# Performance work log

Measured on AMD Instinct MI355X. Metric: run time of the kernel, lower is better.

Reference implementation:

```python
import jax, jax.numpy as jnp
import numpy as np

EPS = 1e-6

def _quant_per_token(x):
    # dynamic per-token symmetric int8 quantization (simulated in float)
    s = jnp.max(jnp.abs(x), axis=-1, keepdims=True) / 127.0  # [T,1]
    q = jnp.clip(jnp.round(x / s), -127.0, 127.0)
    return q, s

def _quant_weight(W):
    # per-output-channel symmetric int8 weight quantization (W: [out,in])
    s = jnp.max(jnp.abs(W), axis=1, keepdims=True) / 127.0  # [out,1]
    q = jnp.round(W / s)
    return q, s

def _w8a8(qx, sx, W, b):
    # int8xint8 GEMM with per-token act scale and per-channel weight scale, fp out
    qw, sw = _quant_weight(W)
    return (qx @ qw.T) * (sx * sw.T) + b

def _rmsnorm_bias(x, w, b, eps=EPS):
    # RMSNormGeneral: x * rsqrt(mean(x^2)+eps) * w + b (no mean subtraction)
    var = jnp.mean(x * x, axis=-1, keepdims=True)
    return x * jax.lax.rsqrt(var + eps) * w + b

def setup_inputs() -> dict:
    key = jax.random.key(0)
    ks = jax.random.split(key, 16)
    E, H, F = 1280, 20, 5120
    B, S = 16, 1024
    T = B * S
    d = {
        'hidden': jax.random.normal(ks[0], (T, E), jnp.float32),
        'ln1_w': jax.random.uniform(ks[1], (E,), jnp.float32, 0.5, 1.5),
        'ln1_b': jax.random.normal(ks[2], (E,), jnp.float32) * 0.02,
        'ln2_w': jax.random.uniform(ks[3], (E,), jnp.float32, 0.5, 1.5),
        'ln2_b': jax.random.normal(ks[4], (E,), jnp.float32) * 0.02,
        'W_qkv': jax.random.normal(ks[5], (3 * E, E), jnp.float32) * 0.02,
        'b_qkv': jax.random.normal(ks[6], (3 * E,), jnp.float32) * 0.02,
        'W_out': jax.random.normal(ks[7], (E, E), jnp.float32) * 0.02,
        'b_out': jax.random.normal(ks[8], (E,), jnp.float32) * 0.02,
        'W_fc1': jax.random.normal(ks[9], (F, E), jnp.float32) * 0.02,
        'b_fc1': jax.random.normal(ks[10], (F,), jnp.float32) * 0.02,
        'W_fc2': jax.random.normal(ks[11], (E, F), jnp.float32) * 0.02,
        'b_fc2': jax.random.normal(ks[12], (E,), jnp.float32) * 0.02,
        'bsz': B,
        'seqlen': S,
    }
    return d

def reference(hidden, ln1_w, ln1_b, ln2_w, ln2_b, W_qkv, b_qkv, W_out, b_out,
              W_fc1, b_fc1, W_fc2, b_fc2, bsz, seqlen):
    E = hidden.shape[-1]
    H = 20
    hd = E // H

    # --- self-attention block ---
    residual = hidden
    y = _rmsnorm_bias(hidden, ln1_w, ln1_b)
    qx, sx = _quant_per_token(y)
    qkv = _w8a8(qx, sx, W_qkv, b_qkv)                      # [T, 3E]
    q, k, v = jnp.split(qkv, 3, axis=-1)
    q = q.reshape(bsz, seqlen, H, hd)
    k = k.reshape(bsz, seqlen, H, hd)
    v = v.reshape(bsz, seqlen, H, hd)
    scale = 1.0 / np.sqrt(hd)
    scores = jnp.einsum('bqhd,bkhd->bhqk', q, k) * scale   # non-causal
    probs = jax.nn.softmax(scores, axis=-1)
    attn = jnp.einsum('bhqk,bkhd->bqhd', probs, v).reshape(bsz * seqlen, E)
    qa, sa = _quant_per_token(attn)
    o = _w8a8(qa, sa, W_out, b_out)
    hidden = residual + o

    # --- MLP block ---
    residual = hidden
    y = _rmsnorm_bias(hidden, ln2_w, ln2_b)
    qx, sx = _quant_per_token(y)
    f1 = _w8a8(qx, sx, W_fc1, b_fc1)                       # [T, F]
    g = jax.nn.gelu(f1, approximate=False)                 # fused gelu_and_quant
    qg, sg = _quant_per_token(g)
    f2 = _w8a8(qg, sg, W_fc2, b_fc2)
    return residual + f2
```

## Files before the change

### kernel.cpp

```cpp
#include <hip/hip_runtime.h>
#include <hip/hip_bf16.h>
#include <stdint.h>

#define E_DIM 1280
#define F_DIM 5120
#define T_DIM 16384
#define B_SZ  16
#define S_LEN 1024
#define NH    20

typedef int v4i __attribute__((ext_vector_type(4)));
typedef __attribute__((ext_vector_type(8))) short v8s;
typedef __attribute__((ext_vector_type(4))) float v4f;

__device__ __forceinline__ float wred_sum(float v) {
#pragma unroll
  for (int m = 32; m > 0; m >>= 1) v += __shfl_xor(v, m, 64);
  return v;
}
__device__ __forceinline__ float wred_max(float v) {
#pragma unroll
  for (int m = 32; m > 0; m >>= 1) v = fmaxf(v, __shfl_xor(v, m, 64));
  return v;
}
__device__ __forceinline__ void gload_lds16(const void* g, void* l) {
  __builtin_amdgcn_global_load_lds((const __attribute__((address_space(1))) void*)g,
                                   (__attribute__((address_space(3))) void*)l, 16, 0, 0);
}

__global__ __launch_bounds__(256) void wquant_kernel(
    const float* __restrict__ W, int8_t* __restrict__ qw, float* __restrict__ sw, int K) {
  __shared__ float red[4];
  const int row = blockIdx.x;
  const int tid = threadIdx.x;
  const float* wr = W + (size_t)row * K;
  float amax = 0.f;
  for (int c = tid; c < K; c += 256) amax = fmaxf(amax, fabsf(wr[c]));
  amax = wred_max(amax);
  if ((tid & 63) == 0) red[tid >> 6] = amax;
  __syncthreads();
  amax = fmaxf(fmaxf(red[0], red[1]), fmaxf(red[2], red[3]));
  float sc = amax * (1.0f / 127.0f);
  if (tid == 0) sw[row] = sc;
  for (int c = tid; c < K; c += 256) {
    float qv = rintf(wr[c] / sc);
    qw[(size_t)row * K + c] = (int8_t)qv;
  }
}

__global__ __launch_bounds__(256) void rms_quant_kernel(
    const float* __restrict__ x, const float* __restrict__ w, const float* __restrict__ b,
    int8_t* __restrict__ q, float* __restrict__ s) {
  __shared__ float red[4];
  const int row = blockIdx.x;
  const int tid = threadIdx.x;
  const float* xr = x + (size_t)row * E_DIM;
  float vals[5];
  float ss = 0.f;
#pragma unroll
  for (int i = 0; i < 5; ++i) {
    float v = xr[tid + i * 256];
    vals[i] = v; ss += v * v;
  }
  ss = wred_sum(ss);
  if ((tid & 63) == 0) red[tid >> 6] = ss;
  __syncthreads();
  ss = red[0] + red[1] + red[2] + red[3];
  float rstd = rsqrtf(ss * (1.0f / E_DIM) + 1e-6f);
  float y[5]; float amax = 0.f;
#pragma unroll
  for (int i = 0; i < 5; ++i) {
    int c = tid + i * 256;
    float v = vals[i] * rstd * w[c] + b[c];
    y[i] = v;
    amax = fmaxf(amax, fabsf(v));
  }
  amax = wred_max(amax);
  __syncthreads();
  if ((tid & 63) == 0) red[tid >> 6] = amax;
  __syncthreads();
  amax = fmaxf(fmaxf(red[0], red[1]), fmaxf(red[2], red[3]));
  float sc = amax * (1.0f / 127.0f);
  if (tid == 0) s[row] = sc;
#pragma unroll
  for (int i = 0; i < 5; ++i) {
    int c = tid + i * 256;
    float qv = rintf(y[i] / sc);
    qv = fminf(fmaxf(qv, -127.f), 127.f);
    q[(size_t)row * E_DIM + c] = (int8_t)qv;
  }
}

__global__ __launch_bounds__(256) void row_quant_bf_kernel(
    const __hip_bfloat16* __restrict__ x, int8_t* __restrict__ q, float* __restrict__ s) {
  __shared__ float red[4];
  const int row = blockIdx.x;
  const int tid = threadIdx.x;
  const __hip_bfloat16* xr = x + (size_t)row * E_DIM;
  float vals[5]; float amax = 0.f;
#pragma unroll
  for (int i = 0; i < 5; ++i) {
    float v = __bfloat162float(xr[tid + i * 256]);
    vals[i] = v;
    amax = fmaxf(amax, fabsf(v));
  }
  amax = wred_max(amax);
  if ((tid & 63) == 0) red[tid >> 6] = amax;
  __syncthreads();
  amax = fmaxf(fmaxf(red[0], red[1]), fmaxf(red[2], red[3]));
  float sc = amax * (1.0f / 127.0f);
  if (tid == 0) s[row] = sc;
#pragma unroll
  for (int i = 0; i < 5; ++i) {
    int c = tid + i * 256;
    float qv = rintf(vals[i] / sc);
    qv = fminf(fmaxf(qv, -127.f), 127.f);
    q[(size_t)row * E_DIM + c] = (int8_t)qv;
  }
}

__global__ __launch_bounds__(256) void gelu_quant_kernel(
    const __hip_bfloat16* __restrict__ f1, int8_t* __restrict__ q, float* __restrict__ s) {
  __shared__ float red[4];
  const int row = blockIdx.x;
  const int tid = threadIdx.x;
  const __hip_bfloat16* xr = f1 + (size_t)row * F_DIM;
  float g[20]; float amax = 0.f;
#pragma unroll
  for (int i = 0; i < 20; ++i) {
    float v = __bfloat162float(xr[tid + i * 256]);
    float gv = 0.5f * v * (1.0f + erff(v * 0.70710678118654752440f));
    g[i] = gv;
    amax = fmaxf(amax, fabsf(gv));
  }
  amax = wred_max(amax);
  if ((tid & 63) == 0) red[tid >> 6] = amax;
  __syncthreads();
  amax = fmaxf(fmaxf(red[0], red[1]), fmaxf(red[2], red[3]));
  float sc = amax * (1.0f / 127.0f);
  if (tid == 0) s[row] = sc;
  int8_t* qr = q + (size_t)row * (2 * F_DIM);
#pragma unroll
  for (int i = 0; i < 20; ++i) {
    int c = tid + i * 256;
    float qv = rintf(g[i] / sc);
    qv = fminf(fmaxf(qv, -127.f), 127.f);
    qr[c] = (int8_t)qv;
  }
}

template <int MODE>
__global__ __launch_bounds__(256) void gemm_i8(
    const int8_t* __restrict__ A, const int8_t* __restrict__ B,
    const float* __restrict__ sx, const float* __restrict__ sw,
    const float* __restrict__ bias, const float* __restrict__ resid,
    void* __restrict__ outp, int M, int N, int K, int lda) {
  __shared__ __align__(16) int8_t Asl[128 * 64];
  __shared__ __align__(16) int8_t Bsl[128 * 64];
  const int tid = threadIdx.x;
  const int lane = tid & 63;
  const int wave = tid >> 6;
  const int wm = wave >> 1, wn = wave & 1;
  const int quad = lane >> 4;
  const int l16 = lane & 15;
  const int m0 = blockIdx.y * 128;
  const int n0 = blockIdx.x * 128;

  v4i acc[4][4];
#pragma unroll
  for (int i = 0; i < 4; ++i)
#pragma unroll
    for (int j = 0; j < 4; ++j) acc[i][j] = (v4i){0, 0, 0, 0};

  const int nk = K >> 6;
#pragma unroll 1
  for (int ks = 0; ks < nk; ++ks) {
    __syncthreads();
    const long k0 = (long)ks * 64;
#pragma unroll
    for (int issue = 0; issue < 2; ++issue) {
      int c = (issue * 4 + wave) * 64 + lane;
      int row = c >> 2;
      int scol = (c & 3) << 4;
      int gcol = scol ^ ((row & 3) << 4);
      gload_lds16(A + (long)(m0 + row) * lda + k0 + gcol, &Asl[c * 16]);
      gload_lds16(B + (long)(n0 + row) * K + k0 + gcol, &Bsl[c * 16]);
    }
    __syncthreads();
    v4i af[4], bf[4];
#pragma unroll
    for (int i = 0; i < 4; ++i) {
      int row = wm * 64 + i * 16 + l16;
      af[i] = *(const v4i*)&Asl[row * 64 + ((quad * 16) ^ ((row & 3) << 4))];
    }
#pragma unroll
    for (int j = 0; j < 4; ++j) {
      int row = wn * 64 + j * 16 + l16;
      bf[j] = *(const v4i*)&Bsl[row * 64 + ((quad * 16) ^ ((row & 3) << 4))];
    }
#pragma unroll
    for (int i = 0; i < 4; ++i)
#pragma unroll
      for (int j = 0; j < 4; ++j)
        acc[i][j] = __builtin_amdgcn_mfma_i32_16x16x64_i8(af[i], bf[j], acc[i][j], 0, 0, 0);
  }

  float swv[4], bv[4];
#pragma unroll
  for (int j = 0; j < 4; ++j) {
    int n = n0 + wn * 64 + j * 16 + l16;
    swv[j] = sw[n];
    bv[j] = bias[n];
  }
#pragma unroll
  for (int i = 0; i < 4; ++i) {
#pragma unroll
    for (int r = 0; r < 4; ++r) {
      int m = m0 + wm * 64 + i * 16 + quad * 4 + r;
      float sxm = sx[m];
#pragma unroll
      for (int j = 0; j < 4; ++j) {
        int n = n0 + wn * 64 + j * 16 + l16;
        float v = (float)acc[i][j][r] * (sxm * swv[j]) + bv[j];
        if constexpr (MODE == 0) {
          ((__hip_bfloat16*)outp)[(size_t)m * N + n] = __float2bfloat16(v);
        } else {
          ((float*)outp)[(size_t)m * N + n] = v + resid[(size_t)m * N + n];
        }
      }
    }
  }
}

__global__ __launch_bounds__(256) void vt_kernel(
    const __hip_bfloat16* __restrict__ qkv, __hip_bfloat16* __restrict__ Vt) {
  __shared__ __hip_bfloat16 tile[64][72];
  const int bh = blockIdx.y, kc = blockIdx.x;
  const int b = bh / NH, h = bh % NH;
  const int tid = threadIdx.x;
  const size_t base = ((size_t)b * S_LEN + (size_t)kc * 64) * (3 * E_DIM) + 2 * E_DIM + h * 64;
#pragma unroll
  for (int i = 0; i < 2; ++i) {
    int idx = tid + i * 256;
    int row = idx >> 3, c8 = (idx & 7) * 8;
    *(uint4*)&tile[row][c8] = *(const uint4*)(qkv + base + (size_t)row * (3 * E_DIM) + c8);
  }
  __syncthreads();
#pragma unroll
  for (int i = 0; i < 2; ++i) {
    int idx = tid + i * 256;
    int d = idx >> 3, k8 = (idx & 7) * 8;
    __hip_bfloat16 v[8] __attribute__((aligned(16)));
#pragma unroll
    for (int j = 0; j < 8; ++j) v[j] = tile[k8 + j][d];
    *(uint4*)&Vt[((size_t)bh * 64 + d) * 1024 + (size_t)kc * 64 + k8] = *(uint4*)v;
  }
}

__global__ __launch_bounds__(256) void attn_flash_kernel(
    const __hip_bfloat16* __restrict__ qkv, const __hip_bfloat16* __restrict__ Vt,
    __hip_bfloat16* __restrict__ attn) {
  constexpr int E3 = 3 * E_DIM;
  __shared__ __align__(16) __hip_bfloat16 Ks[128 * 64];
  __shared__ __align__(16) __hip_bfloat16 Vs[64 * 128];
  __shared__ __align__(16) __hip_bfloat16 Ps[4][16 * 128];
  __shared__ float stats[4][16];

  const int tid = threadIdx.x;
  const int lane = tid & 63;
  const int wave = tid >> 6;
  const int l16 = lane & 15;
  const int quad = lane >> 4;
  const int bh = blockIdx.y;
  const int b = bh / NH, h = bh % NH;
  const int q0 = blockIdx.x * 64;
  const size_t base_t = (size_t)b * S_LEN;

  v8s qb0, qb1;
  {
    const __hip_bfloat16* qp =
        qkv + (base_t + q0 + wave * 16 + l16) * (size_t)E3 + h * 64 + quad * 8;
    qb0 = *(const v8s*)qp;
    qb1 = *(const v8s*)(qp + 32);
  }

  float m_prev = -3.0e38f;
  float lsum = 0.f;
  v4f oc[4];
#pragma unroll
  for (int dt = 0; dt < 4; ++dt) oc[dt] = (v4f){0.f, 0.f, 0.f, 0.f};

  const __hip_bfloat16* kgbase = qkv + base_t * E3 + E_DIM + h * 64;
  const __hip_bfloat16* vgbase = Vt + (size_t)bh * 64 * 1024;
  __hip_bfloat16* pw = Ps[wave];

#pragma unroll 1
  for (int t = 0; t < 8; ++t) {
    __syncthreads();
#pragma unroll
    for (int i = 0; i < 4; ++i) {
      int c = tid + i * 256;
      int row = c >> 3, lc = c & 7;
      int gc = lc ^ (row & 7);
      gload_lds16(kgbase + (size_t)(t * 128 + row) * E3 + gc * 8, (char*)Ks + c * 16);
    }
#pragma unroll
    for (int i = 0; i < 4; ++i) {
      int c = tid + i * 256;
      int d = c >> 4, lc = c & 15;
      int gc = lc ^ (d & 15);
      gload_lds16(vgbase + (size_t)d * 1024 + t * 128 + gc * 8, (char*)Vs + c * 16);
    }
    __syncthreads();

    v4f accT[8];
#pragma unroll
    for (int nt = 0; nt < 8; ++nt) {
      int row = nt * 16 + l16;
      const char* kr = (const char*)Ks + row * 128;
      v8s ak0 = *(const v8s*)(kr + ((quad ^ (row & 7)) * 16));
      v8s ak1 = *(const v8s*)(kr + (((quad + 4) ^ (row & 7)) * 16));
      v4f z = {0.f, 0.f, 0.f, 0.f};
      z = __builtin_amdgcn_mfma_f32_16x16x32_bf16(ak0, qb0, z, 0, 0, 0);
      accT[nt] = __builtin_amdgcn_mfma_f32_16x16x32_bf16(ak1, qb1, accT[nt] = z, 0, 0, 0);
    }

    float mt = -3.0e38f;
#pragma unroll
    for (int nt = 0; nt < 8; ++nt)
#pragma unroll
      for (int r = 0; r < 4; ++r) mt = fmaxf(mt, accT[nt][r]);
    mt = fmaxf(mt, __shfl_xor(mt, 16, 64));
    mt = fmaxf(mt, __shfl_xor(mt, 32, 64));
    float m_new = fmaxf(m_prev, mt);
    float alpha = __expf(0.125f * (m_prev - m_new));
    m_prev = m_new;
    float ts = 0.f;
#pragma unroll
    for (int nt = 0; nt < 8; ++nt)
#pragma unroll
      for (int r = 0; r < 4; ++r) {
        float e = __expf(0.125f * (accT[nt][r] - m_new));
        accT[nt][r] = e;
        ts += e;
      }
    lsum = lsum * alpha + ts;
    if (quad == 0) stats[wave][l16] = alpha;
#pragma unroll
    for (int nt = 0; nt < 8; ++nt) {
      __hip_bfloat16 pk[4] __attribute__((aligned(8)));
#pragma unroll
      for (int r = 0; r < 4; ++r) pk[r] = __float2bfloat16(accT[nt][r]);
      int lcq = 2 * nt + (quad >> 1);
      *(uint2*)((char*)pw + l16 * 256 + ((lcq ^ l16) * 16) + (quad & 1) * 8) = *(uint2*)pk;
    }
    v4f a4 = *(v4f*)&stats[wave][quad * 4];
#pragma unroll
    for (int dt = 0; dt < 4; ++dt)
#pragma unroll
      for (int r = 0; r < 4; ++r) oc[dt][r] *= a4[r];
#pragma unroll
    for (int ks = 0; ks < 4; ++ks) {
      int pch = (ks * 4 + quad) ^ l16;
      v8s ap = *(const v8s*)((char*)pw + l16 * 256 + pch * 16);
#pragma unroll
      for (int dt = 0; dt < 4; ++dt) {
        int d = dt * 16 + l16;
        v8s bv = *(const v8s*)((char*)Vs + d * 256 + (((ks * 4 + quad) ^ l16) * 16));
        oc[dt] = __builtin_amdgcn_mfma_f32_16x16x32_bf16(ap, bv, oc[dt], 0, 0, 0);
      }
    }
  }

  lsum += __shfl_xor(lsum, 16, 64);
  lsum += __shfl_xor(lsum, 32, 64);
  if (quad == 0) stats[wave][l16] = lsum;
  v4f l4 = *(v4f*)&stats[wave][quad * 4];
  float inv[4];
#pragma unroll
  for (int r = 0; r < 4; ++r) inv[r] = 1.0f / l4[r];
#pragma unroll
  for (int dt = 0; dt < 4; ++dt)
#pragma unroll
    for (int r = 0; r < 4; ++r) {
      int tok = q0 + wave * 16 + quad * 4 + r;
      attn[(base_t + tok) * (size_t)E_DIM + h * 64 + dt * 16 + l16] =
          __float2bfloat16(oc[dt][r] * inv[r]);
    }
}

extern "C" void kernel_launch(void* const* d_in, const int* in_sizes, int n_in,
                              void* d_out, int out_size, void* d_ws, size_t ws_size,
                              hipStream_t stream) {
  const float* hidden = (const float*)d_in[0];
  const float* ln1_w = (const float*)d_in[1];
  const float* ln1_b = (const float*)d_in[2];
  const float* ln2_w = (const float*)d_in[3];
  const float* ln2_b = (const float*)d_in[4];
  const float* W_qkv = (const float*)d_in[5];
  const float* b_qkv = (const float*)d_in[6];
  const float* W_out = (const float*)d_in[7];
  const float* b_out = (const float*)d_in[8];
  const float* W_fc1 = (const float*)d_in[9];
  const float* b_fc1 = (const float*)d_in[10];
  const float* W_fc2 = (const float*)d_in[11];
  const float* b_fc2 = (const float*)d_in[12];

  char* ws = (char*)d_ws;
  size_t off = 0;
  auto alloc = [&](size_t bytes) {
    void* p = ws + off;
    off += (bytes + 255) & ~(size_t)255;
    return p;
  };
  int8_t* qw_qkv = (int8_t*)alloc((size_t)3 * E_DIM * E_DIM);
  int8_t* qw_out = (int8_t*)alloc((size_t)E_DIM * E_DIM);
  int8_t* qw_fc1 = (int8_t*)alloc((size_t)F_DIM * E_DIM);
  int8_t* qw_fc2 = (int8_t*)alloc((size_t)E_DIM * F_DIM);
  float* sw_qkv = (float*)alloc((size_t)3 * E_DIM * 4);
  float* sw_out = (float*)alloc((size_t)E_DIM * 4);
  float* sw_fc1 = (float*)alloc((size_t)F_DIM * 4);
  float* sw_fc2 = (float*)alloc((size_t)E_DIM * 4);
  float* sx1 = (float*)alloc((size_t)T_DIM * 4);
  float* sa  = (float*)alloc((size_t)T_DIM * 4);
  float* sx2 = (float*)alloc((size_t)T_DIM * 4);
  float* sg  = (float*)alloc((size_t)T_DIM * 4);
  int8_t* qx = (int8_t*)alloc((size_t)T_DIM * E_DIM);
  char* R = (char*)alloc((size_t)T_DIM * 3 * E_DIM * 2 +
                         (size_t)T_DIM * E_DIM * 4);
  __hip_bfloat16* qkv_bf = (__hip_bfloat16*)R;
  __hip_bfloat16* attn_bf = (__hip_bfloat16*)(R + (size_t)T_DIM * 3 * E_DIM * 2);
  __hip_bfloat16* Vt = (__hip_bfloat16*)(R + (size_t)T_DIM * 3 * E_DIM * 2 +
                                         (size_t)T_DIM * E_DIM * 2);
  __hip_bfloat16* f1_bf = (__hip_bfloat16*)R;
  int8_t* qg = (int8_t*)R;
  float* hidden2 = (float*)d_out;

  wquant_kernel<<<3 * E_DIM, 256, 0, stream>>>(W_qkv, qw_qkv, sw_qkv, E_DIM);
  wquant_kernel<<<E_DIM, 256, 0, stream>>>(W_out, qw_out, sw_out, E_DIM);
  wquant_kernel<<<F_DIM, 256, 0, stream>>>(W_fc1, qw_fc1, sw_fc1, E_DIM);
  wquant_kernel<<<E_DIM, 256, 0, stream>>>(W_fc2, qw_fc2, sw_fc2, F_DIM);
  rms_quant_kernel<<<T_DIM, 256, 0, stream>>>(hidden, ln1_w, ln1_b, qx, sx1);
  gemm_i8<0><<<dim3(3 * E_DIM / 128, T_DIM / 128), 256, 0, stream>>>(
      qx, qw_qkv, sx1, sw_qkv, b_qkv, nullptr, qkv_bf, T_DIM, 3 * E_DIM, E_DIM, E_DIM);
  vt_kernel<<<dim3(S_LEN / 64, B_SZ * NH), 256, 0, stream>>>(qkv_bf, Vt);
  attn_flash_kernel<<<dim3(S_LEN / 64, B_SZ * NH), 256, 0, stream>>>(qkv_bf, Vt, attn_bf);
  row_quant_bf_kernel<<<T_DIM, 256, 0, stream>>>(attn_bf, qx, sa);
  gemm_i8<1><<<dim3(E_DIM / 128, T_DIM / 128), 256, 0, stream>>>(
      qx, qw_out, sa, sw_out, b_out, hidden, hidden2, T_DIM, E_DIM, E_DIM, E_DIM);
  rms_quant_kernel<<<T_DIM, 256, 0, stream>>>(hidden2, ln2_w, ln2_b, qx, sx2);
  gemm_i8<0><<<dim3(F_DIM / 128, T_DIM / 128), 256, 0, stream>>>(
      qx, qw_fc1, sx2, sw_fc1, b_fc1, nullptr, f1_bf, T_DIM, F_DIM, E_DIM, E_DIM);
  gelu_quant_kernel<<<T_DIM, 256, 0, stream>>>(f1_bf, qg, sg);
  gemm_i8<1><<<dim3(E_DIM / 128, T_DIM / 128), 256, 0, stream>>>(
      qg, qw_fc2, sg, sw_fc2, b_fc2, hidden2, (float*)d_out, T_DIM, E_DIM, F_DIM, 2 * F_DIM);
}
```

Before: 1.155 ms.

## Replace int8 GEMM with 256x256 double-buffered pipelined kernel and XCD-aware tile mapping

Replaces the 128x128 single-buffered int8 GEMM with a 256x256-tile, 8-wave kernel. It double-buffers two 64-wide K slices in LDS and interleaves the next slice's global-to-LDS loads with MFMA phases, using s_setprio and explicit vmcnt waits. A block-index remap spreads tiles across XCDs, and a new LDS swizzle avoids bank conflicts. This aims to hide load latency and raise data reuse per tile, at the cost of 128KB of LDS per block, a larger register footprint and fewer tiles for the narrow-N GEMMs.

```diff
diff --git a/kernel.cpp b/kernel.cpp
--- a/kernel.cpp
+++ b/kernel.cpp
@@ -150,78 +150,148 @@
 }
 
 template <int MODE>
-__global__ __launch_bounds__(256) void gemm_i8(
+__global__ __launch_bounds__(512, 2) void gemm256_i8(
     const int8_t* __restrict__ A, const int8_t* __restrict__ B,
     const float* __restrict__ sx, const float* __restrict__ sw,
     const float* __restrict__ bias, const float* __restrict__ resid,
     void* __restrict__ outp, int M, int N, int K, int lda) {
-  __shared__ __align__(16) int8_t Asl[128 * 64];
-  __shared__ __align__(16) int8_t Bsl[128 * 64];
+  __shared__ __align__(16) int8_t As[2][2][256 * 64];
+  __shared__ __align__(16) int8_t Bs[2][2][256 * 64];
+
   const int tid = threadIdx.x;
   const int lane = tid & 63;
   const int wave = tid >> 6;
-  const int wm = wave >> 1, wn = wave & 1;
+  const int wm = wave >> 2;
+  const int wn = wave & 3;
+  const int l16 = lane & 15;
   const int quad = lane >> 4;
-  const int l16 = lane & 15;
-  const int m0 = blockIdx.y * 128;
-  const int n0 = blockIdx.x * 128;
-
-  v4i acc[4][4];
-#pragma unroll
-  for (int i = 0; i < 4; ++i)
+  const int choff = (quad ^ ((l16 >> 1) & 3)) << 4;
+
+  const int nwg = gridDim.x;
+  const int ntn = N >> 8;
+  const int u = (blockIdx.x & 7) * (nwg >> 3) + (blockIdx.x >> 3);
+  const int tm = u / ntn, tn = u % ntn;
+  const int m0 = tm << 8, n0 = tn << 8;
+
+  const int8_t* A_blk = A + (size_t)m0 * lda;
+  const int8_t* B_blk = B + (size_t)n0 * K;
+
+  const int r0 = tid >> 2;
+  const int sch = ((tid & 3) ^ ((tid >> 3) & 3)) << 4;
+
+#define STAGE_A(KT, DST)                                                         \
+  {                                                                              \
+    gload_lds16(A_blk + (size_t)r0 * lda + (size_t)(KT)*64 + sch,                \
+                (DST) + tid * 16);                                               \
+    gload_lds16(A_blk + (size_t)(r0 + 128) * lda + (size_t)(KT)*64 + sch,        \
+                (DST) + 8192 + tid * 16);                                        \
+  }
+#define STAGE_B(KT, DST)                                                         \
+  {                                                                              \
+    gload_lds16(B_blk + (size_t)r0 * K + (size_t)(KT)*64 + sch,                  \
+                (DST) + tid * 16);                                               \
+    gload_lds16(B_blk + (size_t)(r0 + 128) * K + (size_t)(KT)*64 + sch,          \
+                (DST) + 8192 + tid * 16);                                        \
+  }
+
+  v4i acc[8][4];
+#pragma unroll
+  for (int i = 0; i < 8; ++i)
 #pragma unroll
     for (int j = 0; j < 4; ++j) acc[i][j] = (v4i){0, 0, 0, 0};
 
   const int nk = K >> 6;
+  const int niter = nk >> 1;
+
+  STAGE_A(0, &As[0][0][0]); STAGE_B(0, &Bs[0][0][0]);
+  STAGE_A(1, &As[0][1][0]); STAGE_B(1, &Bs[0][1][0]);
+  asm volatile("s_waitcnt vmcnt(4)" ::: "memory");
+  asm volatile("s_barrier" ::: "memory");
+
 #pragma unroll 1
-  for (int ks = 0; ks < nk; ++ks) {
-    __syncthreads();
-    const long k0 = (long)ks * 64;
-#pragma unroll
-    for (int issue = 0; issue < 2; ++issue) {
-      int c = (issue * 4 + wave) * 64 + lane;
-      int row = c >> 2;
-      int scol = (c & 3) << 4;
-      int gcol = scol ^ ((row & 3) << 4);
-      gload_lds16(A + (long)(m0 + row) * lda + k0 + gcol, &Asl[c * 16]);
-      gload_lds16(B + (long)(n0 + row) * K + k0 + gcol, &Bsl[c * 16]);
-    }
-    __syncthreads();
-    v4i af[4], bf[4];
-#pragma unroll
-    for (int i = 0; i < 4; ++i) {
-      int row = wm * 64 + i * 16 + l16;
-      af[i] = *(const v4i*)&Asl[row * 64 + ((quad * 16) ^ ((row & 3) << 4))];
-    }
-#pragma unroll
-    for (int j = 0; j < 4; ++j) {
-      int row = wn * 64 + j * 16 + l16;
-      bf[j] = *(const v4i*)&Bsl[row * 64 + ((quad * 16) ^ ((row & 3) << 4))];
-    }
-#pragma unroll
-    for (int i = 0; i < 4; ++i)
-#pragma unroll
-      for (int j = 0; j < 4; ++j)
-        acc[i][j] = __builtin_amdgcn_mfma_i32_16x16x64_i8(af[i], bf[j], acc[i][j], 0, 0, 0);
-  }
+  for (int i = 0; i < niter - 1; ++i) {
+    const int pr = i & 1;
+    const int kt2 = 2 * i + 2;
+#pragma unroll
+    for (int ph = 0; ph < 4; ++ph) {
+      const int tt = ph >> 1;
+      const int qm = ph & 1;
+      const int8_t* At = &As[pr][tt][0];
+      const int8_t* Bt = &Bs[pr][tt][0];
+      v4i af[4], bf[4];
+#pragma unroll
+      for (int ii = 0; ii < 4; ++ii)
+        af[ii] = *(const v4i*)(At + (wm * 128 + qm * 64 + ii * 16 + l16) * 64 + choff);
+#pragma unroll
+      for (int jj = 0; jj < 4; ++jj)
+        bf[jj] = *(const v4i*)(Bt + (wn * 64 + jj * 16 + l16) * 64 + choff);
+      if (qm == 0) {
+        STAGE_A(kt2 + tt, &As[pr ^ 1][tt][0]);
+      } else {
+        STAGE_B(kt2 + tt, &Bs[pr ^ 1][tt][0]);
+      }
+      asm volatile("s_barrier" ::: "memory");
+      __builtin_amdgcn_s_setprio(1);
+#pragma unroll
+      for (int ii = 0; ii < 4; ++ii)
+#pragma unroll
+        for (int jj = 0; jj < 4; ++jj)
+          acc[qm * 4 + ii][jj] = __builtin_amdgcn_mfma_i32_16x16x64_i8(
+              af[ii], bf[jj], acc[qm * 4 + ii][jj], 0, 0, 0);
+      __builtin_amdgcn_s_setprio(0);
+      if (qm == 1) asm volatile("s_waitcnt vmcnt(4)" ::: "memory");
+      asm volatile("s_barrier" ::: "memory");
+    }
+  }
+
+  {
+    const int pr = (niter - 1) & 1;
+#pragma unroll
+    for (int ph = 0; ph < 4; ++ph) {
+      const int tt = ph >> 1;
+      const int qm = ph & 1;
+      const int8_t* At = &As[pr][tt][0];
+      const int8_t* Bt = &Bs[pr][tt][0];
+      v4i af[4], bf[4];
+#pragma unroll
+      for (int ii = 0; ii < 4; ++ii)
+        af[ii] = *(const v4i*)(At + (wm * 128 + qm * 64 + ii * 16 + l16) * 64 + choff);
+#pragma unroll
+      for (int jj = 0; jj < 4; ++jj)
+        bf[jj] = *(const v4i*)(Bt + (wn * 64 + jj * 16 + l16) * 64 + choff);
+      asm volatile("s_barrier" ::: "memory");
+      __builtin_amdgcn_s_setprio(1);
+#pragma unroll
+      for (int ii = 0; ii < 4; ++ii)
+#pragma unroll
+        for (int jj = 0; jj < 4; ++jj)
+          acc[qm * 4 + ii][jj] = __builtin_amdgcn_mfma_i32_16x16x64_i8(
+              af[ii], bf[jj], acc[qm * 4 + ii][jj], 0, 0, 0);
+      __builtin_amdgcn_s_setprio(0);
+      if (ph == 1) asm volatile("s_waitcnt vmcnt(0)" ::: "memory");
+      asm volatile("s_barrier" ::: "memory");
+    }
+  }
+#undef STAGE_A
+#undef STAGE_B
 
   float swv[4], bv[4];
 #pragma unroll
-  for (int j = 0; j < 4; ++j) {
-    int n = n0 + wn * 64 + j * 16 + l16;
-    swv[j] = sw[n];
-    bv[j] = bias[n];
-  }
-#pragma unroll
-  for (int i = 0; i < 4; ++i) {
+  for (int jj = 0; jj < 4; ++jj) {
+    int n = n0 + wn * 64 + jj * 16 + l16;
+    swv[jj] = sw[n];
+    bv[jj] = bias[n];
+  }
+#pragma unroll
+  for (int mf = 0; mf < 8; ++mf) {
 #pragma unroll
     for (int r = 0; r < 4; ++r) {
-      int m = m0 + wm * 64 + i * 16 + quad * 4 + r;
+      int m = m0 + wm * 128 + mf * 16 + quad * 4 + r;
       float sxm = sx[m];
 #pragma unroll
-      for (int j = 0; j < 4; ++j) {
-        int n = n0 + wn * 64 + j * 16 + l16;
-        float v = (float)acc[i][j][r] * (sxm * swv[j]) + bv[j];
+      for (int jj = 0; jj < 4; ++jj) {
+        int n = n0 + wn * 64 + jj * 16 + l16;
+        float v = (float)acc[mf][jj][r] * (sxm * swv[jj]) + bv[jj];
         if constexpr (MODE == 0) {
           ((__hip_bfloat16*)outp)[(size_t)m * N + n] = __float2bfloat16(v);
         } else {
@@ -441,17 +511,17 @@
   wquant_kernel<<<F_DIM, 256, 0, stream>>>(W_fc1, qw_fc1, sw_fc1, E_DIM);
   wquant_kernel<<<E_DIM, 256, 0, stream>>>(W_fc2, qw_fc2, sw_fc2, F_DIM);
   rms_quant_kernel<<<T_DIM, 256, 0, stream>>>(hidden, ln1_w, ln1_b, qx, sx1);
-  gemm_i8<0><<<dim3(3 * E_DIM / 128, T_DIM / 128), 256, 0, stream>>>(
+  gemm256_i8<0><<<(T_DIM / 256) * (3 * E_DIM / 256), 512, 0, stream>>>(
       qx, qw_qkv, sx1, sw_qkv, b_qkv, nullptr, qkv_bf, T_DIM, 3 * E_DIM, E_DIM, E_DIM);
   vt_kernel<<<dim3(S_LEN / 64, B_SZ * NH), 256, 0, stream>>>(qkv_bf, Vt);
   attn_flash_kernel<<<dim3(S_LEN / 64, B_SZ * NH), 256, 0, stream>>>(qkv_bf, Vt, attn_bf);
   row_quant_bf_kernel<<<T_DIM, 256, 0, stream>>>(attn_bf, qx, sa);
-  gemm_i8<1><<<dim3(E_DIM / 128, T_DIM / 128), 256, 0, stream>>>(
+  gemm256_i8<1><<<(T_DIM / 256) * (E_DIM / 256), 512, 0, stream>>>(
       qx, qw_out, sa, sw_out, b_out, hidden, hidden2, T_DIM, E_DIM, E_DIM, E_DIM);
   rms_quant_kernel<<<T_DIM, 256, 0, stream>>>(hidden2, ln2_w, ln2_b, qx, sx2);
-  gemm_i8<0><<<dim3(F_DIM / 128, T_DIM / 128), 256, 0, stream>>>(
+  gemm256_i8<0><<<(T_DIM / 256) * (F_DIM / 256), 512, 0, stream>>>(
       qx, qw_fc1, sx2, sw_fc1, b_fc1, nullptr, f1_bf, T_DIM, F_DIM, E_DIM, E_DIM);
   gelu_quant_kernel<<<T_DIM, 256, 0, stream>>>(f1_bf, qg, sg);
-  gemm_i8<1><<<dim3(E_DIM / 128, T_DIM / 128), 256, 0, stream>>>(
+  gemm256_i8<1><<<(T_DIM / 256) * (E_DIM / 256), 512, 0, stream>>>(
       qg, qw_fc2, sg, sw_fc2, b_fc2, hidden2, (float*)d_out, T_DIM, E_DIM, F_DIM, 2 * F_DIM);
 }
```

New measurement: 1.136 ms. About the same (-1.6%).
